# Performance work log

Measured on AMD Instinct MI355X. Metric: run time of the kernel, lower is better.

## Reference

```python
import jax, jax.numpy as jnp
from jax import lax
import numpy as np

WINDOW = 51
HALF = WINDOW // 2  # 25
K_SAUVOLA = 0.2     # skimage threshold_sauvola default k
RGB_W = np.array([0.2989, 0.5870, 0.1140], dtype=np.float32)  # tf.image.rgb_to_grayscale weights


def _window_sum(x, axis):
    """Sliding-window sum of length WINDOW along `axis`, 'same' size, reflect padding.
    O(1) per pixel via cumulative sums (integral-image style), matching the
    uniform_filter-based local statistics in skimage's Sauvola."""
    pad = [(0, 0)] * x.ndim
    pad[axis] = (HALF, HALF)
    xp = jnp.pad(x, pad, mode='reflect')
    cs = jnp.cumsum(xp, axis=axis)
    zshape = list(cs.shape)
    zshape[axis] = 1
    cs = jnp.concatenate([jnp.zeros(zshape, cs.dtype), cs], axis=axis)
    n = cs.shape[axis]
    hi = lax.slice_in_dim(cs, WINDOW, n, axis=axis)
    lo = lax.slice_in_dim(cs, 0, n - WINDOW, axis=axis)
    return hi - lo


def _box_mean(x):
    # separable 51x51 box filter over H (axis 1) and W (axis 2)
    s = _window_sum(_window_sum(x, axis=1), axis=2)
    return s / jnp.asarray(WINDOW * WINDOW, x.dtype)


def setup_inputs() -> dict:
    key = jax.random.key(0)
    inputs = jax.random.uniform(key, (8, 1024, 1024, 3), dtype=jnp.float32)
    return {"inputs": inputs}


def reference(inputs) -> jnp.ndarray:
    # RGB -> grayscale (channels == 3 branch), keep channel dim [B,H,W,1]
    gray = jnp.einsum('bhwc,c->bhw', inputs, jnp.asarray(RGB_W))[..., None]
    # local mean / std over 51x51 window
    m = _box_mean(gray)
    m2 = _box_mean(gray * gray)
    var = jnp.maximum(m2 - m * m, 0.0)
    s = jnp.sqrt(var)
    # skimage default dynamic range: r = 0.5 * (max - min) over the whole array
    r = 0.5 * (jnp.max(gray) - jnp.min(gray))
    thresh = m * (1.0 + K_SAUVOLA * (s / r - 1.0))
    # (gray > thresh) * 1
    return (gray > thresh).astype(jnp.float32)
```

## Files before the change

### kernel.cpp

```cpp
#include <hip/hip_runtime.h>

#define IMW 1024
#define IMH 1024
#define NB  8
#define HALF 25
#define STRIP 32
#define NCELL 64
#define RPB 4

#define W_R ((double)0.2989f)
#define W_G ((double)0.5870f)
#define W_B ((double)0.1140f)
#define INV_AREA (1.0 / 2601.0)

__device__ __forceinline__ int refl(int i, int n) {
    if (i < 0) i = -i;
    if (i >= n) i = 2 * n - 2 - i;
    return i;
}

__device__ __forceinline__ int swz(int p) { return p + (p >> 5); }

__global__ void k0_init(unsigned* cells) {
    cells[threadIdx.x] = (threadIdx.x < NCELL) ? 0xFFFFFFFFu : 0u;
}

__global__ __launch_bounds__(256) void k1_rowpass(const float* __restrict__ in,
                                                  float2* __restrict__ hp,
                                                  float* __restrict__ gray,
                                                  unsigned* __restrict__ cells) {
    __shared__ float gb[RPB][1056];
    const int t = threadIdx.x;
    const int lane = t & 63, w = t >> 6;
    const int row = blockIdx.x * RPB + w;
    const long long base = (long long)row * IMW;
    const int p0 = lane * 16;

    const float4* p4 = (const float4*)(in + base * 3);
    float lmin = 1e30f, lmax = -1e30f;
    #pragma unroll
    for (int q = 0; q < 4; q++) {
        float4 f0 = p4[12*lane + 3*q + 0];
        float4 f1 = p4[12*lane + 3*q + 1];
        float4 f2 = p4[12*lane + 3*q + 2];
        float g0 = (float)((double)f0.x*W_R + (double)f0.y*W_G + (double)f0.z*W_B);
        float g1 = (float)((double)f0.w*W_R + (double)f1.x*W_G + (double)f1.y*W_B);
        float g2 = (float)((double)f1.z*W_R + (double)f1.w*W_G + (double)f2.x*W_B);
        float g3 = (float)((double)f2.y*W_R + (double)f2.z*W_G + (double)f2.w*W_B);
        int p = p0 + 4*q;
        gb[w][swz(p+0)] = g0; gb[w][swz(p+1)] = g1;
        gb[w][swz(p+2)] = g2; gb[w][swz(p+3)] = g3;
        ((float4*)(gray + base + p0))[q] = make_float4(g0, g1, g2, g3);
        lmin = fminf(lmin, fminf(fminf(g0, g1), fminf(g2, g3)));
        lmax = fmaxf(lmax, fmaxf(fmaxf(g0, g1), fmaxf(g2, g3)));
    }

    for (int off = 32; off; off >>= 1) {
        lmin = fminf(lmin, __shfl_down(lmin, off));
        lmax = fmaxf(lmax, __shfl_down(lmax, off));
    }
    if (lane == 0) {
        int cell = row & (NCELL - 1);
        atomicMin(&cells[cell], __float_as_uint(lmin));
        atomicMax(&cells[NCELL + cell], __float_as_uint(lmax));
    }

    __syncthreads();

    double s1a = 0.0, s1b = 0.0, s1c = 0.0;
    double s2a = 0.0, s2b = 0.0, s2c = 0.0;
    #pragma unroll
    for (int i = 0; i < 51; i += 3) {
        double d0 = (double)gb[w][swz(refl(p0 - HALF + i + 0, IMW))];
        double d1 = (double)gb[w][swz(refl(p0 - HALF + i + 1, IMW))];
        double d2 = (double)gb[w][swz(refl(p0 - HALF + i + 2, IMW))];
        s1a += d0; s2a = fma(d0, d0, s2a);
        s1b += d1; s2b = fma(d1, d1, s2b);
        s1c += d2; s2c = fma(d2, d2, s2c);
    }
    double v1 = (s1a + s1b) + s1c;
    double v2 = (s2a + s2b) + s2c;

    float4* hp4 = (float4*)(hp + base + p0);
    float hx0 = 0.f, hy0 = 0.f;
    #pragma unroll
    for (int j = 0; j < 16; j++) {
        float hx = (float)v1, hy = (float)v2;
        if (j & 1) hp4[j >> 1] = make_float4(hx0, hy0, hx, hy);
        else { hx0 = hx; hy0 = hy; }
        if (j != 15) {
            int p = p0 + j;
            double ga = (double)gb[w][swz(refl(p + HALF + 1, IMW))];
            double gs = (double)gb[w][swz(refl(p - HALF,     IMW))];
            v1 += ga - gs;
            v2 += ga * ga - gs * gs;
        }
    }
}

__global__ __launch_bounds__(256) void k2_colpass(const float* __restrict__ gray,
                                                  const float2* __restrict__ hp,
                                                  const unsigned* __restrict__ cells,
                                                  float* __restrict__ out) {
    __shared__ double sr[2];
    const int t = threadIdx.x;
    if (t < 64) {
        unsigned mn = cells[t];
        unsigned mx = cells[NCELL + t];
        for (int off = 32; off; off >>= 1) {
            unsigned a = __shfl_down(mn, off);
            unsigned b = __shfl_down(mx, off);
            mn = (a < mn) ? a : mn;
            mx = (b > mx) ? b : mx;
        }
        if (t == 0) {
            sr[0] = (double)__uint_as_float(mn);
            sr[1] = (double)__uint_as_float(mx);
        }
    }
    __syncthreads();
    const double r  = 0.5 * (sr[1] - sr[0]);
    const double r2 = r * r;

    const int id   = blockIdx.x;
    const int b    = id & 7;
    const int rest = id >> 3;
    const int ys   = rest & 31;
    const int xc   = rest >> 5;
    const int x  = xc * 256 + t;
    const int y0 = ys * STRIP;
    const long long ib = (long long)b * IMH * IMW;

    double vx = 0.0, vy = 0.0;
    #pragma unroll 8
    for (int j = -HALF; j <= HALF; j++) {
        int ry = refl(y0 + j, IMH);
        float2 h = hp[ib + (long long)ry * IMW + x];
        vx += (double)h.x; vy += (double)h.y;
    }

    #pragma unroll 8
    for (int y = y0; y < y0 + STRIP; y++) {
        long long pix = ib + (long long)y * IMW + x;
        double g = (double)gray[pix];

        double m  = vx * INV_AREA;
        double va = fmax(vy * INV_AREA - m * m, 0.0);
        double A  = g - 0.8 * m;
        int o = (A > 0.0) && (A * A * r2 > 0.04 * m * m * va);
        out[pix] = o ? 1.0f : 0.0f;

        int ra = refl(y + HALF + 1, IMH);
        int rs = refl(y - HALF, IMH);
        float2 ha = hp[ib + (long long)ra * IMW + x];
        float2 hs = hp[ib + (long long)rs * IMW + x];
        vx += (double)ha.x - (double)hs.x;
        vy += (double)ha.y - (double)hs.y;
    }
}

extern "C" void kernel_launch(void* const* d_in, const int* in_sizes, int n_in,
                              void* d_out, int out_size, void* d_ws, size_t ws_size,
                              hipStream_t stream) {
    const float* in = (const float*)d_in[0];
    float* out = (float*)d_out;

    unsigned* cells = (unsigned*)d_ws;
    float2* hp = (float2*)((char*)d_ws + 4096);
    float* gray = (float*)((char*)d_ws + 4096
                           + (size_t)NB * IMH * IMW * sizeof(float2));

    hipLaunchKernelGGL(k0_init, dim3(1), dim3(2 * NCELL), 0, stream, cells);
    hipLaunchKernelGGL(k1_rowpass, dim3(NB * IMH / RPB), dim3(256), 0, stream,
                       in, hp, gray, cells);
    hipLaunchKernelGGL(k2_colpass, dim3((IMW / 256) * (IMH / STRIP) * NB), dim3(256), 0, stream,
                       gray, hp, cells, out);
}
```

Baseline: 228.0 us.

## Fuse horizontal and vertical box passes into a tiled shared-memory kernel

The row-pass intermediate buffer (float2 per pixel, written to and reread from global memory) is removed. The first kernel now only computes grayscale and per-block min/max. The second kernel loads a 64x32 output tile plus a 25-pixel halo of gray rows, computes horizontal window sums into LDS, then runs vertical sliding sums per column to produce the threshold. This trades global traffic for redundant halo recomputation and lower parallelism, since only 164 threads do the horizontal pass and each uses a large register array.

```diff
diff --git a/kernel.cpp b/kernel.cpp
--- a/kernel.cpp
+++ b/kernel.cpp
@@ -4,9 +4,10 @@
 #define IMH 1024
 #define NB  8
 #define HALF 25
-#define STRIP 32
+#define TW 64
+#define TH 32
+#define HBR (TH + 2*HALF)
 #define NCELL 64
-#define RPB 4
 
 #define W_R ((double)0.2989f)
 #define W_G ((double)0.5870f)
@@ -25,137 +26,150 @@
     cells[threadIdx.x] = (threadIdx.x < NCELL) ? 0xFFFFFFFFu : 0u;
 }
 
-__global__ __launch_bounds__(256) void k1_rowpass(const float* __restrict__ in,
-                                                  float2* __restrict__ hp,
-                                                  float* __restrict__ gray,
-                                                  unsigned* __restrict__ cells) {
-    __shared__ float gb[RPB][1056];
+__global__ __launch_bounds__(256) void k1_gray(const float* __restrict__ in,
+                                               float* __restrict__ gray,
+                                               unsigned* __restrict__ cells) {
+    __shared__ float bmin[4], bmax[4];
     const int t = threadIdx.x;
     const int lane = t & 63, w = t >> 6;
-    const int row = blockIdx.x * RPB + w;
-    const long long base = (long long)row * IMW;
-    const int p0 = lane * 16;
+    const long long gt = (long long)blockIdx.x * 256 + t;
 
-    const float4* p4 = (const float4*)(in + base * 3);
-    float lmin = 1e30f, lmax = -1e30f;
-    #pragma unroll
-    for (int q = 0; q < 4; q++) {
-        float4 f0 = p4[12*lane + 3*q + 0];
-        float4 f1 = p4[12*lane + 3*q + 1];
-        float4 f2 = p4[12*lane + 3*q + 2];
-        float g0 = (float)((double)f0.x*W_R + (double)f0.y*W_G + (double)f0.z*W_B);
-        float g1 = (float)((double)f0.w*W_R + (double)f1.x*W_G + (double)f1.y*W_B);
-        float g2 = (float)((double)f1.z*W_R + (double)f1.w*W_G + (double)f2.x*W_B);
-        float g3 = (float)((double)f2.y*W_R + (double)f2.z*W_G + (double)f2.w*W_B);
-        int p = p0 + 4*q;
-        gb[w][swz(p+0)] = g0; gb[w][swz(p+1)] = g1;
-        gb[w][swz(p+2)] = g2; gb[w][swz(p+3)] = g3;
-        ((float4*)(gray + base + p0))[q] = make_float4(g0, g1, g2, g3);
-        lmin = fminf(lmin, fminf(fminf(g0, g1), fminf(g2, g3)));
-        lmax = fmaxf(lmax, fmaxf(fmaxf(g0, g1), fmaxf(g2, g3)));
-    }
+    const float4* p4 = (const float4*)in + 3 * gt;
+    float4 f0 = p4[0], f1 = p4[1], f2 = p4[2];
+    float g0 = (float)((double)f0.x*W_R + (double)f0.y*W_G + (double)f0.z*W_B);
+    float g1 = (float)((double)f0.w*W_R + (double)f1.x*W_G + (double)f1.y*W_B);
+    float g2 = (float)((double)f1.z*W_R + (double)f1.w*W_G + (double)f2.x*W_B);
+    float g3 = (float)((double)f2.y*W_R + (double)f2.z*W_G + (double)f2.w*W_B);
+    ((float4*)gray)[gt] = make_float4(g0, g1, g2, g3);
 
+    float lmin = fminf(fminf(g0, g1), fminf(g2, g3));
+    float lmax = fmaxf(fmaxf(g0, g1), fmaxf(g2, g3));
     for (int off = 32; off; off >>= 1) {
         lmin = fminf(lmin, __shfl_down(lmin, off));
         lmax = fmaxf(lmax, __shfl_down(lmax, off));
     }
-    if (lane == 0) {
-        int cell = row & (NCELL - 1);
-        atomicMin(&cells[cell], __float_as_uint(lmin));
-        atomicMax(&cells[NCELL + cell], __float_as_uint(lmax));
-    }
-
+    if (lane == 0) { bmin[w] = lmin; bmax[w] = lmax; }
     __syncthreads();
-
-    double s1a = 0.0, s1b = 0.0, s1c = 0.0;
-    double s2a = 0.0, s2b = 0.0, s2c = 0.0;
-    #pragma unroll
-    for (int i = 0; i < 51; i += 3) {
-        double d0 = (double)gb[w][swz(refl(p0 - HALF + i + 0, IMW))];
-        double d1 = (double)gb[w][swz(refl(p0 - HALF + i + 1, IMW))];
-        double d2 = (double)gb[w][swz(refl(p0 - HALF + i + 2, IMW))];
-        s1a += d0; s2a = fma(d0, d0, s2a);
-        s1b += d1; s2b = fma(d1, d1, s2b);
-        s1c += d2; s2c = fma(d2, d2, s2c);
-    }
-    double v1 = (s1a + s1b) + s1c;
-    double v2 = (s2a + s2b) + s2c;
-
-    float4* hp4 = (float4*)(hp + base + p0);
-    float hx0 = 0.f, hy0 = 0.f;
-    #pragma unroll
-    for (int j = 0; j < 16; j++) {
-        float hx = (float)v1, hy = (float)v2;
-        if (j & 1) hp4[j >> 1] = make_float4(hx0, hy0, hx, hy);
-        else { hx0 = hx; hy0 = hy; }
-        if (j != 15) {
-            int p = p0 + j;
-            double ga = (double)gb[w][swz(refl(p + HALF + 1, IMW))];
-            double gs = (double)gb[w][swz(refl(p - HALF,     IMW))];
-            v1 += ga - gs;
-            v2 += ga * ga - gs * gs;
-        }
+    if (t == 0) {
+        float m0 = fminf(fminf(bmin[0], bmin[1]), fminf(bmin[2], bmin[3]));
+        float m1 = fmaxf(fmaxf(bmax[0], bmax[1]), fmaxf(bmax[2], bmax[3]));
+        int cell = blockIdx.x & (NCELL - 1);
+        atomicMin(&cells[cell], __float_as_uint(m0));
+        atomicMax(&cells[NCELL + cell], __float_as_uint(m1));
     }
 }
 
-__global__ __launch_bounds__(256) void k2_colpass(const float* __restrict__ gray,
-                                                  const float2* __restrict__ hp,
-                                                  const unsigned* __restrict__ cells,
-                                                  float* __restrict__ out) {
+__global__ __launch_bounds__(256) void k2_fused(const float* __restrict__ gray,
+                                                const unsigned* __restrict__ cells,
+                                                float* __restrict__ out) {
+    __shared__ float h1b[5412], h2b[5412];
     __shared__ double sr[2];
     const int t = threadIdx.x;
+
     if (t < 64) {
         unsigned mn = cells[t];
         unsigned mx = cells[NCELL + t];
         for (int off = 32; off; off >>= 1) {
             unsigned a = __shfl_down(mn, off);
-            unsigned b = __shfl_down(mx, off);
+            unsigned b2 = __shfl_down(mx, off);
             mn = (a < mn) ? a : mn;
-            mx = (b > mx) ? b : mx;
+            mx = (b2 > mx) ? b2 : mx;
         }
         if (t == 0) {
             sr[0] = (double)__uint_as_float(mn);
             sr[1] = (double)__uint_as_float(mx);
         }
     }
-    __syncthreads();
-    const double r  = 0.5 * (sr[1] - sr[0]);
-    const double r2 = r * r;
 
     const int id   = blockIdx.x;
     const int b    = id & 7;
     const int rest = id >> 3;
-    const int ys   = rest & 31;
-    const int xc   = rest >> 5;
-    const int x  = xc * 256 + t;
-    const int y0 = ys * STRIP;
+    const int yt   = rest & 31;
+    const int xt   = rest >> 5;
+    const int x0 = xt * TW, y0 = yt * TH;
     const long long ib = (long long)b * IMH * IMW;
 
-    double vx = 0.0, vy = 0.0;
-    #pragma unroll 8
-    for (int j = -HALF; j <= HALF; j++) {
-        int ry = refl(y0 + j, IMH);
-        float2 h = hp[ib + (long long)ry * IMW + x];
-        vx += (double)h.x; vy += (double)h.y;
+    if (t < 2 * HBR) {
+        const int r  = t >> 1;
+        const int hh = t & 1;
+        const int grow = refl(y0 + r - HALF, IMH);
+        const float* grp = gray + ib + (long long)grow * IMW;
+        const int c0 = x0 + 32 * hh;
+
+        float gr[88];
+        if (x0 == 0 || x0 == IMW - TW) {
+            #pragma unroll
+            for (int i = 0; i < 88; i++) gr[i] = grp[refl(c0 - 28 + i, IMW)];
+        } else {
+            const float4* q = (const float4*)(grp + (c0 - 28));
+            #pragma unroll
+            for (int i = 0; i < 22; i++) {
+                float4 f = q[i];
+                gr[4*i+0] = f.x; gr[4*i+1] = f.y; gr[4*i+2] = f.z; gr[4*i+3] = f.w;
+            }
+        }
+
+        double s1a = 0, s1b = 0, s1c = 0, s2a = 0, s2b = 0, s2c = 0;
+        #pragma unroll
+        for (int i = 3; i < 54; i += 3) {
+            double d0 = (double)gr[i], d1 = (double)gr[i+1], d2 = (double)gr[i+2];
+            s1a += d0; s2a = fma(d0, d0, s2a);
+            s1b += d1; s2b = fma(d1, d1, s2b);
+            s1c += d2; s2c = fma(d2, d2, s2c);
+        }
+        double v1 = (s1a + s1b) + s1c;
+        double v2 = (s2a + s2b) + s2c;
+
+        const int hbase = 32 * t;
+        #pragma unroll
+        for (int j = 0; j < 32; j++) {
+            h1b[swz(hbase + j)] = (float)v1;
+            h2b[swz(hbase + j)] = (float)v2;
+            if (j != 31) {
+                double ga = (double)gr[j + 54], gs = (double)gr[j + 3];
+                v1 += ga - gs;
+                v2 += ga * ga - gs * gs;
+            }
+        }
     }
+    __syncthreads();
 
-    #pragma unroll 8
-    for (int y = y0; y < y0 + STRIP; y++) {
-        long long pix = ib + (long long)y * IMW + x;
-        double g = (double)gray[pix];
+    const double r  = 0.5 * (sr[1] - sr[0]);
+    const double r2 = r * r;
+    const int c  = t & 63;
+    const int g4 = t >> 6;
+    const int r0 = 8 * g4;
 
-        double m  = vx * INV_AREA;
-        double va = fmax(vy * INV_AREA - m * m, 0.0);
-        double A  = g - 0.8 * m;
+    double u1a = 0, u1b = 0, u1c = 0, u2a = 0, u2b = 0, u2c = 0;
+    #pragma unroll
+    for (int i = 0; i < 51; i += 3) {
+        double a0 = (double)h1b[swz((r0 + i    ) * 64 + c)];
+        double a1 = (double)h1b[swz((r0 + i + 1) * 64 + c)];
+        double a2 = (double)h1b[swz((r0 + i + 2) * 64 + c)];
+        u1a += a0; u1b += a1; u1c += a2;
+        double b0 = (double)h2b[swz((r0 + i    ) * 64 + c)];
+        double b1 = (double)h2b[swz((r0 + i + 1) * 64 + c)];
+        double b2 = (double)h2b[swz((r0 + i + 2) * 64 + c)];
+        u2a += b0; u2b += b1; u2c += b2;
+    }
+    double u1 = (u1a + u1b) + u1c;
+    double u2 = (u2a + u2b) + u2c;
+
+    #pragma unroll
+    for (int j = 0; j < 8; j++) {
+        const int yy = y0 + r0 + j;
+        const long long pix = ib + (long long)yy * IMW + (x0 + c);
+        double gv = (double)gray[pix];
+        double m  = u1 * INV_AREA;
+        double va = fmax(u2 * INV_AREA - m * m, 0.0);
+        double A  = gv - 0.8 * m;
         int o = (A > 0.0) && (A * A * r2 > 0.04 * m * m * va);
         out[pix] = o ? 1.0f : 0.0f;
-
-        int ra = refl(y + HALF + 1, IMH);
-        int rs = refl(y - HALF, IMH);
-        float2 ha = hp[ib + (long long)ra * IMW + x];
-        float2 hs = hp[ib + (long long)rs * IMW + x];
-        vx += (double)ha.x - (double)hs.x;
-        vy += (double)ha.y - (double)hs.y;
+        if (j != 7) {
+            const int rr = r0 + j;
+            u1 += (double)h1b[swz((rr + 51) * 64 + c)] - (double)h1b[swz(rr * 64 + c)];
+            u2 += (double)h2b[swz((rr + 51) * 64 + c)] - (double)h2b[swz(rr * 64 + c)];
+        }
     }
 }
 
@@ -166,13 +180,11 @@
     float* out = (float*)d_out;
 
     unsigned* cells = (unsigned*)d_ws;
-    float2* hp = (float2*)((char*)d_ws + 4096);
-    float* gray = (float*)((char*)d_ws + 4096
-                           + (size_t)NB * IMH * IMW * sizeof(float2));
+    float* gray = (float*)((char*)d_ws + 4096);
 
     hipLaunchKernelGGL(k0_init, dim3(1), dim3(2 * NCELL), 0, stream, cells);
-    hipLaunchKernelGGL(k1_rowpass, dim3(NB * IMH / RPB), dim3(256), 0, stream,
-                       in, hp, gray, cells);
-    hipLaunchKernelGGL(k2_colpass, dim3((IMW / 256) * (IMH / STRIP) * NB), dim3(256), 0, stream,
-                       gray, hp, cells, out);
+    hipLaunchKernelGGL(k1_gray, dim3(NB * IMH * IMW / 1024), dim3(256), 0, stream,
+                       in, gray, cells);
+    hipLaunchKernelGGL(k2_fused, dim3(NB * (IMH / TH) * (IMW / TW)), dim3(256), 0, stream,
+                       gray, cells, out);
 }
```

Result: slower. 277.1 us (+21.5%).

## Process one row per block with four pixels per thread in row pass

Applied to the files above, without the earlier changes.

Restructures the horizontal pass so each block handles a single image row and each of 256 threads computes 4 pixels instead of 16 per lane across 4 rows. This aims to improve load coalescing and parallelism and to shorten per-thread serial sliding. In exchange, each thread recomputes the full 51-tap initial window for fewer outputs, which raises fp64 arithmetic and LDS reads per pixel.

```diff
diff --git a/kernel.cpp b/kernel.cpp
--- a/kernel.cpp
+++ b/kernel.cpp
@@ -6,7 +6,6 @@
 #define HALF 25
 #define STRIP 32
 #define NCELL 64
-#define RPB 4
 
 #define W_R ((double)0.2989f)
 #define W_G ((double)0.5870f)
@@ -29,51 +28,44 @@
                                                   float2* __restrict__ hp,
                                                   float* __restrict__ gray,
                                                   unsigned* __restrict__ cells) {
-    __shared__ float gb[RPB][1056];
+    __shared__ float gb[1056];
     const int t = threadIdx.x;
     const int lane = t & 63, w = t >> 6;
-    const int row = blockIdx.x * RPB + w;
+    const int row = blockIdx.x;
     const long long base = (long long)row * IMW;
-    const int p0 = lane * 16;
+    const int p0 = 4 * t;
 
     const float4* p4 = (const float4*)(in + base * 3);
-    float lmin = 1e30f, lmax = -1e30f;
-    #pragma unroll
-    for (int q = 0; q < 4; q++) {
-        float4 f0 = p4[12*lane + 3*q + 0];
-        float4 f1 = p4[12*lane + 3*q + 1];
-        float4 f2 = p4[12*lane + 3*q + 2];
-        float g0 = (float)((double)f0.x*W_R + (double)f0.y*W_G + (double)f0.z*W_B);
-        float g1 = (float)((double)f0.w*W_R + (double)f1.x*W_G + (double)f1.y*W_B);
-        float g2 = (float)((double)f1.z*W_R + (double)f1.w*W_G + (double)f2.x*W_B);
-        float g3 = (float)((double)f2.y*W_R + (double)f2.z*W_G + (double)f2.w*W_B);
-        int p = p0 + 4*q;
-        gb[w][swz(p+0)] = g0; gb[w][swz(p+1)] = g1;
-        gb[w][swz(p+2)] = g2; gb[w][swz(p+3)] = g3;
-        ((float4*)(gray + base + p0))[q] = make_float4(g0, g1, g2, g3);
-        lmin = fminf(lmin, fminf(fminf(g0, g1), fminf(g2, g3)));
-        lmax = fmaxf(lmax, fmaxf(fmaxf(g0, g1), fmaxf(g2, g3)));
-    }
+    float4 f0 = p4[3*t], f1 = p4[3*t+1], f2 = p4[3*t+2];
+    float g0 = (float)((double)f0.x*W_R + (double)f0.y*W_G + (double)f0.z*W_B);
+    float g1 = (float)((double)f0.w*W_R + (double)f1.x*W_G + (double)f1.y*W_B);
+    float g2 = (float)((double)f1.z*W_R + (double)f1.w*W_G + (double)f2.x*W_B);
+    float g3 = (float)((double)f2.y*W_R + (double)f2.z*W_G + (double)f2.w*W_B);
 
+    gb[swz(p0+0)] = g0; gb[swz(p0+1)] = g1;
+    gb[swz(p0+2)] = g2; gb[swz(p0+3)] = g3;
+    ((float4*)(gray + base))[t] = make_float4(g0, g1, g2, g3);
+
+    float lmin = fminf(fminf(g0, g1), fminf(g2, g3));
+    float lmax = fmaxf(fmaxf(g0, g1), fmaxf(g2, g3));
     for (int off = 32; off; off >>= 1) {
         lmin = fminf(lmin, __shfl_down(lmin, off));
         lmax = fmaxf(lmax, __shfl_down(lmax, off));
     }
     if (lane == 0) {
-        int cell = row & (NCELL - 1);
+        int cell = (4 * row + w) & (NCELL - 1);
         atomicMin(&cells[cell], __float_as_uint(lmin));
         atomicMax(&cells[NCELL + cell], __float_as_uint(lmax));
     }
 
     __syncthreads();
 
-    double s1a = 0.0, s1b = 0.0, s1c = 0.0;
-    double s2a = 0.0, s2b = 0.0, s2c = 0.0;
+    double s1a = 0, s1b = 0, s1c = 0, s2a = 0, s2b = 0, s2c = 0;
     #pragma unroll
     for (int i = 0; i < 51; i += 3) {
-        double d0 = (double)gb[w][swz(refl(p0 - HALF + i + 0, IMW))];
-        double d1 = (double)gb[w][swz(refl(p0 - HALF + i + 1, IMW))];
-        double d2 = (double)gb[w][swz(refl(p0 - HALF + i + 2, IMW))];
+        double d0 = (double)gb[swz(refl(p0 - HALF + i + 0, IMW))];
+        double d1 = (double)gb[swz(refl(p0 - HALF + i + 1, IMW))];
+        double d2 = (double)gb[swz(refl(p0 - HALF + i + 2, IMW))];
         s1a += d0; s2a = fma(d0, d0, s2a);
         s1b += d1; s2b = fma(d1, d1, s2b);
         s1c += d2; s2c = fma(d2, d2, s2c);
@@ -81,21 +73,29 @@
     double v1 = (s1a + s1b) + s1c;
     double v2 = (s2a + s2b) + s2c;
 
-    float4* hp4 = (float4*)(hp + base + p0);
-    float hx0 = 0.f, hy0 = 0.f;
-    #pragma unroll
-    for (int j = 0; j < 16; j++) {
-        float hx = (float)v1, hy = (float)v2;
-        if (j & 1) hp4[j >> 1] = make_float4(hx0, hy0, hx, hy);
-        else { hx0 = hx; hy0 = hy; }
-        if (j != 15) {
-            int p = p0 + j;
-            double ga = (double)gb[w][swz(refl(p + HALF + 1, IMW))];
-            double gs = (double)gb[w][swz(refl(p - HALF,     IMW))];
-            v1 += ga - gs;
-            v2 += ga * ga - gs * gs;
-        }
+    float4 h01, h23;
+    h01.x = (float)v1; h01.y = (float)v2;
+    {
+        double ga = (double)gb[swz(refl(p0 + 26, IMW))];
+        double gs = (double)gb[swz(refl(p0 - 25, IMW))];
+        v1 += ga - gs; v2 += ga * ga - gs * gs;
+        h01.z = (float)v1; h01.w = (float)v2;
     }
+    {
+        double ga = (double)gb[swz(refl(p0 + 27, IMW))];
+        double gs = (double)gb[swz(refl(p0 - 24, IMW))];
+        v1 += ga - gs; v2 += ga * ga - gs * gs;
+        h23.x = (float)v1; h23.y = (float)v2;
+    }
+    {
+        double ga = (double)gb[swz(refl(p0 + 28, IMW))];
+        double gs = (double)gb[swz(refl(p0 - 23, IMW))];
+        v1 += ga - gs; v2 += ga * ga - gs * gs;
+        h23.z = (float)v1; h23.w = (float)v2;
+    }
+    float4* o = (float4*)(hp + base + p0);
+    o[0] = h01;
+    o[1] = h23;
 }
 
 __global__ __launch_bounds__(256) void k2_colpass(const float* __restrict__ gray,
@@ -171,7 +171,7 @@
                            + (size_t)NB * IMH * IMW * sizeof(float2));
 
     hipLaunchKernelGGL(k0_init, dim3(1), dim3(2 * NCELL), 0, stream, cells);
-    hipLaunchKernelGGL(k1_rowpass, dim3(NB * IMH / RPB), dim3(256), 0, stream,
+    hipLaunchKernelGGL(k1_rowpass, dim3(NB * IMH), dim3(256), 0, stream,
                        in, hp, gray, cells);
     hipLaunchKernelGGL(k2_colpass, dim3((IMW / 256) * (IMH / STRIP) * NB), dim3(256), 0, stream,
                        gray, hp, cells, out);
```

After: 317.6 us. 39.3% more time.
